# Performance work log

Hardware: AMD Instinct MI355X
Metric: run time of the kernel (lower is better)

Reference implementation:

```python
import jax, jax.numpy as jnp
import numpy as np

NUM_HEADS = 16

def setup_inputs() -> dict:
    key = jax.random.key(0)
    ks = jax.random.split(key, 6)
    C = 512
    nW, B, N = 64, 4, 144
    x = jax.random.normal(ks[0], (B * nW, N, C), dtype=jnp.float32)
    mask = jax.random.randint(ks[1], (nW, N, N), 0, 2, dtype=jnp.int32)
    Wqkv = jax.random.normal(ks[2], (C, 3 * C), dtype=jnp.float32) * (1.0 / np.sqrt(C))
    bqkv = jnp.zeros((3 * C,), dtype=jnp.float32)
    Wproj = jax.random.normal(ks[3], (C, C), dtype=jnp.float32) * (1.0 / np.sqrt(C))
    bproj = jnp.zeros((C,), dtype=jnp.float32)
    return {"x": x, "mask": mask, "Wqkv": Wqkv, "bqkv": bqkv, "Wproj": Wproj, "bproj": bproj}

def reference(x, mask, Wqkv, bqkv, Wproj, bproj):
    Bn, N, C = x.shape
    H = NUM_HEADS
    D = C // H
    nW = mask.shape[0]
    B = Bn // nW
    scale = 1.0 / jnp.sqrt(jnp.asarray(D, dtype=x.dtype))

    qkv = x @ Wqkv + bqkv                        # (Bn, N, 3C)
    qkv = qkv.reshape(Bn, N, 3, H, D)            # packed order (qkv, H, D)
    qkv = jnp.transpose(qkv, (2, 0, 3, 1, 4))    # (3, Bn, H, N, D)
    q, k, v = qkv[0], qkv[1], qkv[2]

    # split window-batch dim: (B nW) -> B, nW
    q = q.reshape(B, nW, H, N, D)
    k = k.reshape(B, nW, H, N, D)
    v = v.reshape(B, nW, H, N, D)

    attn = jnp.einsum('bwhnd,bwhmd->bwhnm', q, k) * scale
    bias = jnp.where(mask == 0, -jnp.inf, 0.0).astype(x.dtype)  # (nW, N, N)
    attn = attn + bias.reshape(1, nW, 1, N, N)
    attn = jax.nn.softmax(attn, axis=-1)

    out = jnp.einsum('bwhnm,bwhmd->bwhnd', attn, v)   # (B, nW, H, N, D)
    out = jnp.transpose(out, (0, 1, 3, 2, 4)).reshape(Bn, N, C)
    return out @ Wproj + bproj
```

## Files before the change

kernel.cpp:

```cpp
#include <hip/hip_runtime.h>

typedef unsigned short u16;
typedef unsigned int u32;
typedef __attribute__((ext_vector_type(4))) float f32x4;
typedef __attribute__((ext_vector_type(8))) short bf16x8;
typedef __attribute__((ext_vector_type(4))) u32 u32x4;

__device__ __forceinline__ u16 f2bf(float f) {
  union { float f; u32 u; } v; v.f = f;
  u32 r = v.u + 0x7fffu + ((v.u >> 16) & 1u);
  return (u16)(r >> 16);
}

__device__ __forceinline__ u16 f2bf_rne(float f) {
  u32 w;
  asm("v_cvt_pk_bf16_f32 %0, %1, %2" : "=v"(w) : "v"(f), "v"(f));
  return (u16)w;
}

__device__ __forceinline__ void gload_lds16(const u16* g, u16* l) {
  __builtin_amdgcn_global_load_lds((__attribute__((address_space(1))) const void*)g,
                                   (__attribute__((address_space(3))) void*)l,
                                   16, 0, 0);
}

__global__ void __launch_bounds__(256) k_transpose_w(const float* __restrict__ W,
                                                     u16* __restrict__ Wt, int K, int Nc) {
  __shared__ u16 t[64][72];
  const int tid = threadIdx.x;
  const int kb = blockIdx.x * 64, nb = blockIdx.y * 64;
  const int c4 = (tid & 15) * 4;
  const int r0 = tid >> 4;
#pragma unroll
  for (int rr = 0; rr < 4; ++rr) {
    int r = rr * 16 + r0;
    float4 v = *(const float4*)(W + (size_t)(kb + r) * Nc + nb + c4);
    t[r][c4 + 0] = f2bf(v.x);
    t[r][c4 + 1] = f2bf(v.y);
    t[r][c4 + 2] = f2bf(v.z);
    t[r][c4 + 3] = f2bf(v.w);
  }
  __syncthreads();
  const int c8 = (tid & 7) * 8;
  const int rn = tid >> 3;
#pragma unroll
  for (int rr = 0; rr < 2; ++rr) {
    int n = rr * 32 + rn;
    u16 tmp[8];
#pragma unroll
    for (int j = 0; j < 8; ++j) tmp[j] = t[c8 + j][n];
    *(u32x4*)(Wt + (size_t)(nb + n) * K + kb + c8) = *(const u32x4*)tmp;
  }
}

__global__ void k_mask_bits(const int* __restrict__ mask, u32* __restrict__ mtab) {
  int idx = blockIdx.x * blockDim.x + threadIdx.x;
  if (idx >= 64 * 144 * 8) return;
  int wd = idx & 7;
  int r = idx >> 3;
  u32 bits = 0;
  if (wd < 5) {
    int base = r * 144 + wd * 32;
    int nmax = 144 - wd * 32;
    if (nmax > 32) nmax = 32;
    for (int b = 0; b < nmax; ++b) bits |= (mask[base + b] ? 1u : 0u) << b;
  }
  mtab[idx] = bits;
}

template <bool OUT_BF16, bool A_FP32>
__global__ void __launch_bounds__(256, 3) k_gemm(const void* __restrict__ Ap,
                                                 const u16* __restrict__ Bt,
                                                 const float* __restrict__ bias,
                                                 void* __restrict__ D,
                                                 int Nc, int K, int NB) {
  __shared__ u16 As[128 * 68];
  __shared__ u16 Bs[2][128 * 64];
  const int tid = threadIdx.x;
  const int wave = tid >> 6, lane = tid & 63;
  const int wr = wave >> 1, wc = wave & 1;
  const int l15 = lane & 15, g = lane >> 4;
  const int sx = l15 & 7;
  const f32x4 fzero = {0.f, 0.f, 0.f, 0.f};

  const int cpx = gridDim.x >> 3;
  const int swz = (blockIdx.x & 7) * cpx + (blockIdx.x >> 3);
  const int bm = swz / NB, bn = swz % NB;

  const u16* Bb = Bt + (size_t)bn * 128 * K;

  int rr[4], cc[4];
#pragma unroll
  for (int i = 0; i < 4; ++i) {
    int e = i * 256 + tid;
    rr[i] = e >> 3;
    cc[i] = e & 7;
  }

  f32x4 acc[4][4];
#pragma unroll
  for (int m = 0; m < 4; ++m)
#pragma unroll
    for (int n = 0; n < 4; ++n) acc[m][n] = fzero;

  f32x4 areg[8];
  u32x4 aregb[4];

  auto A_LOAD = [&](int ks) {
    if constexpr (A_FP32) {
      const float* Af = (const float*)Ap;
#pragma unroll
      for (int i = 0; i < 4; ++i) {
        const float* p = Af + (size_t)(bm * 128 + rr[i]) * K + ks + cc[i] * 8;
        areg[2 * i] = *(const f32x4*)(p);
        areg[2 * i + 1] = *(const f32x4*)(p + 4);
      }
    } else {
      const u16* Ab = (const u16*)Ap + (size_t)bm * 128 * K;
#pragma unroll
      for (int i = 0; i < 4; ++i)
        aregb[i] = *(const u32x4*)(Ab + (size_t)rr[i] * K + ks + cc[i] * 8);
    }
  };

  auto A_WRITE = [&]() {
#pragma unroll
    for (int i = 0; i < 4; ++i) {
      u32x4 wv;
      if constexpr (A_FP32) {
        u32 w0, w1, w2, w3;
        asm("v_cvt_pk_bf16_f32 %0, %1, %2" : "=v"(w0) : "v"(areg[2 * i][0]), "v"(areg[2 * i][1]));
        asm("v_cvt_pk_bf16_f32 %0, %1, %2" : "=v"(w1) : "v"(areg[2 * i][2]), "v"(areg[2 * i][3]));
        asm("v_cvt_pk_bf16_f32 %0, %1, %2" : "=v"(w2) : "v"(areg[2 * i + 1][0]), "v"(areg[2 * i + 1][1]));
        asm("v_cvt_pk_bf16_f32 %0, %1, %2" : "=v"(w3) : "v"(areg[2 * i + 1][2]), "v"(areg[2 * i + 1][3]));
        wv[0] = w0; wv[1] = w1; wv[2] = w2; wv[3] = w3;
      } else {
        wv = aregb[i];
      }
      *(u32x4*)(&As[rr[i] * 68 + cc[i] * 8]) = wv;
    }
  };

  auto B_STAGE = [&](int buf, int ks) {
#pragma unroll
    for (int i = 0; i < 4; ++i) {
      int cs = cc[i] ^ (rr[i] & 7);
      gload_lds16(Bb + (size_t)rr[i] * K + ks + (cs << 3), &Bs[buf][(i * 256 + tid) * 8]);
    }
  };

  auto COMPUTE = [&](int buf) {
#pragma unroll
    for (int kk = 0; kk < 2; ++kk) {
      bf16x8 a[4], b[4];
#pragma unroll
      for (int m = 0; m < 4; ++m)
        a[m] = *(const bf16x8*)(&As[(wr * 64 + m * 16 + l15) * 68 + (kk * 4 + g) * 8]);
#pragma unroll
      for (int n = 0; n < 4; ++n)
        b[n] = *(const bf16x8*)(&Bs[buf][(wc * 64 + n * 16 + l15) * 64 + (((kk * 4 + g) ^ sx) << 3)]);
#pragma unroll
      for (int m = 0; m < 4; ++m)
#pragma unroll
        for (int n = 0; n < 4; ++n)
          acc[m][n] = __builtin_amdgcn_mfma_f32_16x16x32_bf16(a[m], b[n], acc[m][n], 0, 0, 0);
    }
  };

  const int nt = K >> 6;
  A_LOAD(0);
  B_STAGE(0, 0);
  int cur = 0;
  for (int t = 0; t < nt; ++t) {
    asm volatile("s_waitcnt vmcnt(0)" ::: "memory");
    __builtin_amdgcn_sched_barrier(0);
    if (t + 1 < nt) B_STAGE(cur ^ 1, (t + 1) << 6);
    A_WRITE();
    if (t + 1 < nt) A_LOAD((t + 1) << 6);
    asm volatile("s_waitcnt lgkmcnt(0)" ::: "memory");
    __builtin_amdgcn_sched_barrier(0);
    __builtin_amdgcn_s_barrier();
    __builtin_amdgcn_sched_barrier(0);
    COMPUTE(cur);
    __builtin_amdgcn_sched_barrier(0);
    if (t + 1 < nt) __builtin_amdgcn_s_barrier();
    cur ^= 1;
  }

  const int row0 = bm * 128 + wr * 64;
  const int col0 = bn * 128 + wc * 64;
#pragma unroll
  for (int m = 0; m < 4; ++m) {
#pragma unroll
    for (int n = 0; n < 4; ++n) {
      int col = col0 + n * 16 + l15;
      float bv = bias[col];
#pragma unroll
      for (int j = 0; j < 4; ++j) {
        int row = row0 + m * 16 + g * 4 + j;
        float v = acc[m][n][j] + bv;
        if constexpr (OUT_BF16)
          ((u16*)D)[(size_t)row * Nc + col] = f2bf_rne(v);
        else
          ((float*)D)[(size_t)row * Nc + col] = v;
      }
    }
  }
}

__global__ void __launch_bounds__(192) k_attn(const u16* __restrict__ qkv,
                                              const u32* __restrict__ mtab,
                                              u16* __restrict__ obuf) {
  __shared__ u16 k_s[144 * 40];
  __shared__ u16 vT_s[32 * 168];
  __shared__ u16 P_s[3][16 * 168];

  const int bh = blockIdx.x;
  const int bn = bh >> 4, h = bh & 15;
  const int wid = bn & 63;
  const int tid = threadIdx.x;
  const int wave = tid >> 6, lane = tid & 63;
  const int l15 = lane & 15, g = lane >> 4;
  const f32x4 fzero = {0.f, 0.f, 0.f, 0.f};

  const u16* base = qkv + (size_t)bn * 144 * 1536 + h * 32;
  u16* Pw = &P_s[wave][0];

  bf16x8 qb[3];
  u32 mw[3][5];
#pragma unroll
  for (int it = 0; it < 3; ++it) {
    const int mt = wave + it * 3;
    qb[it] = *(const bf16x8*)(base + (size_t)(mt * 16 + l15) * 1536 + g * 8);
    const u32* mp = mtab + ((size_t)(wid * 144 + mt * 16 + l15) << 3);
#pragma unroll
    for (int wd = 0; wd < 5; ++wd) mw[it][wd] = mp[wd];
  }

  *(u32*)(Pw + l15 * 168 + 144 + g * 4) = 0;
  *(u32*)(Pw + l15 * 168 + 144 + g * 4 + 2) = 0;

  for (int e = tid; e < 576; e += 192) {
    int n = e >> 2, c = e & 3;
    const u16* rowp = base + (size_t)n * 1536 + c * 8;
    u32x4 kv = *(const u32x4*)(rowp + 512);
    u32x4 vv = *(const u32x4*)(rowp + 1024);
    *(u32x4*)(k_s + n * 40 + c * 8) = kv;
#pragma unroll
    for (int t = 0; t < 4; ++t) {
      u32 w = vv[t];
      vT_s[(c * 8 + 2 * t) * 168 + n] = (u16)(w & 0xffffu);
      vT_s[(c * 8 + 2 * t + 1) * 168 + n] = (u16)(w >> 16);
    }
  }
  for (int e = tid; e < 512; e += 192) {
    int d = e >> 4, c = e & 15;
    vT_s[d * 168 + 144 + c] = 0;
  }
  __syncthreads();

  const float scale = 0.17677669529663687f;

#pragma unroll
  for (int it = 0; it < 3; ++it) {
    const int mt = wave + it * 3;

    f32x4 accs[9];
#pragma unroll
    for (int nt = 0; nt < 9; ++nt) {
      bf16x8 kf = *(const bf16x8*)(k_s + (nt * 16 + l15) * 40 + g * 8);
      accs[nt] = __builtin_amdgcn_mfma_f32_16x16x32_bf16(kf, qb[it], fzero, 0, 0, 0);
    }

    float rsum = 0.f;
#pragma unroll
    for (int nt = 0; nt < 9; ++nt) {
      const int wd = nt >> 1;
      const int shb = (nt & 1) * 16;
#pragma unroll
      for (int j = 0; j < 4; ++j) {
        float e = __expf(accs[nt][j] * scale);
        u32 bit = (mw[it][wd] >> (shb + g * 4 + j)) & 1u;
        e = bit ? e : 0.f;
        accs[nt][j] = e;
        rsum += e;
      }
    }
    rsum += __shfl_xor(rsum, 16, 64);
    rsum += __shfl_xor(rsum, 32, 64);
    const float rinv = 1.f / rsum;

#pragma unroll
    for (int nt = 0; nt < 9; ++nt) {
      u32 w0, w1;
      float p0 = accs[nt][0] * rinv, p1 = accs[nt][1] * rinv;
      float p2 = accs[nt][2] * rinv, p3 = accs[nt][3] * rinv;
      asm("v_cvt_pk_bf16_f32 %0, %1, %2" : "=v"(w0) : "v"(p0), "v"(p1));
      asm("v_cvt_pk_bf16_f32 %0, %1, %2" : "=v"(w1) : "v"(p2), "v"(p3));
      *(u32*)(Pw + l15 * 168 + nt * 16 + g * 4) = w0;
      *(u32*)(Pw + l15 * 168 + nt * 16 + g * 4 + 2) = w1;
    }

    asm volatile("s_waitcnt lgkmcnt(0)" ::: "memory");
    __builtin_amdgcn_sched_barrier(0);

    f32x4 acco[2];
    acco[0] = fzero;
    acco[1] = fzero;
#pragma unroll
    for (int kk = 0; kk < 5; ++kk) {
      bf16x8 pa = *(const bf16x8*)(Pw + l15 * 168 + kk * 32 + g * 8);
#pragma unroll
      for (int nt2 = 0; nt2 < 2; ++nt2) {
        bf16x8 b = *(const bf16x8*)(vT_s + (nt2 * 16 + l15) * 168 + kk * 32 + g * 8);
        acco[nt2] = __builtin_amdgcn_mfma_f32_16x16x32_bf16(pa, b, acco[nt2], 0, 0, 0);
      }
    }
#pragma unroll
    for (int nt2 = 0; nt2 < 2; ++nt2)
#pragma unroll
      for (int j = 0; j < 4; ++j) {
        int r = mt * 16 + g * 4 + j;
        int d = nt2 * 16 + l15;
        obuf[((size_t)bn * 144 + r) * 512 + h * 32 + d] = f2bf_rne(acco[nt2][j]);
      }
  }
}

extern "C" void kernel_launch(void* const* d_in, const int* in_sizes, int n_in,
                              void* d_out, int out_size, void* d_ws, size_t ws_size,
                              hipStream_t stream) {
  const float* x = (const float*)d_in[0];
  const int* mask = (const int*)d_in[1];
  const float* Wqkv = (const float*)d_in[2];
  const float* bqkv = (const float*)d_in[3];
  const float* Wproj = (const float*)d_in[4];
  const float* bproj = (const float*)d_in[5];
  float* out = (float*)d_out;

  char* ws = (char*)d_ws;
  u32* mtab    = (u32*)(ws + 0);
  u16* wqkv_t  = (u16*)(ws + 294912);
  u16* qkv     = (u16*)(ws + 1867776);
  u16* obuf    = (u16*)(ws + 115113984);
  u16* wproj_t = (u16*)(ws + 152862720);

  k_transpose_w<<<dim3(8, 24), 256, 0, stream>>>(Wqkv, wqkv_t, 512, 1536);
  k_transpose_w<<<dim3(8, 8), 256, 0, stream>>>(Wproj, wproj_t, 512, 512);
  k_mask_bits<<<288, 256, 0, stream>>>(mask, mtab);
  k_gemm<true, true><<<3456, 256, 0, stream>>>(x, wqkv_t, bqkv, qkv, 1536, 512, 12);
  k_attn<<<4096, 192, 0, stream>>>(qkv, mtab, obuf);
  k_gemm<false, false><<<1152, 256, 0, stream>>>(obuf, wproj_t, bproj, out, 512, 512, 4);
}
```

Measured before the change: 196.9 us.

## Use nine waves per attention block and ballot-based mask bit packing

The attention kernel now launches 576 threads (9 waves) per window-head, so each wave handles a single 16-row query tile instead of looping over three. K/V staging is done in one pass, with one row chunk per thread. The mask bitpacking kernel uses wave ballots over rows instead of serial per-thread loops. MFMA priority is raised around the PV product. The larger blocks raise per-block LDS use (9 P buffers), which may limit how many blocks fit per CU.

```diff
diff --git a/kernel.cpp b/kernel.cpp
--- a/kernel.cpp
+++ b/kernel.cpp
@@ -2,6 +2,7 @@
 
 typedef unsigned short u16;
 typedef unsigned int u32;
+typedef unsigned long long u64;
 typedef __attribute__((ext_vector_type(4))) float f32x4;
 typedef __attribute__((ext_vector_type(8))) short bf16x8;
 typedef __attribute__((ext_vector_type(4))) u32 u32x4;
@@ -53,19 +54,21 @@
   }
 }
 
-__global__ void k_mask_bits(const int* __restrict__ mask, u32* __restrict__ mtab) {
-  int idx = blockIdx.x * blockDim.x + threadIdx.x;
-  if (idx >= 64 * 144 * 8) return;
-  int wd = idx & 7;
-  int r = idx >> 3;
-  u32 bits = 0;
-  if (wd < 5) {
-    int base = r * 144 + wd * 32;
-    int nmax = 144 - wd * 32;
-    if (nmax > 32) nmax = 32;
-    for (int b = 0; b < nmax; ++b) bits |= (mask[base + b] ? 1u : 0u) << b;
-  }
-  mtab[idx] = bits;
+__global__ void __launch_bounds__(256) k_mask_bits(const int* __restrict__ mask,
+                                                   u32* __restrict__ mtab) {
+  const int row = blockIdx.x * 4 + (threadIdx.x >> 6);
+  const int lane = threadIdx.x & 63;
+  const int* base = mask + (size_t)row * 144;
+  u64 b01 = __ballot(base[lane] != 0);
+  u64 b23 = __ballot(base[64 + lane] != 0);
+  int v4 = (lane < 16) ? base[128 + lane] : 0;
+  u64 b4 = __ballot(v4 != 0);
+  if (lane == 0) {
+    u32* o = mtab + (size_t)row * 8;
+    o[0] = (u32)b01; o[1] = (u32)(b01 >> 32);
+    o[2] = (u32)b23; o[3] = (u32)(b23 >> 32);
+    o[4] = (u32)b4;  o[5] = 0; o[6] = 0; o[7] = 0;
+  }
 }
 
 template <bool OUT_BF16, bool A_FP32>
@@ -208,12 +211,12 @@
   }
 }
 
-__global__ void __launch_bounds__(192) k_attn(const u16* __restrict__ qkv,
+__global__ void __launch_bounds__(576) k_attn(const u16* __restrict__ qkv,
                                               const u32* __restrict__ mtab,
                                               u16* __restrict__ obuf) {
   __shared__ u16 k_s[144 * 40];
   __shared__ u16 vT_s[32 * 168];
-  __shared__ u16 P_s[3][16 * 168];
+  __shared__ u16 P_s[9][16 * 168];
 
   const int bh = blockIdx.x;
   const int bn = bh >> 4, h = bh & 15;
@@ -225,23 +228,19 @@
 
   const u16* base = qkv + (size_t)bn * 144 * 1536 + h * 32;
   u16* Pw = &P_s[wave][0];
-
-  bf16x8 qb[3];
-  u32 mw[3][5];
-#pragma unroll
-  for (int it = 0; it < 3; ++it) {
-    const int mt = wave + it * 3;
-    qb[it] = *(const bf16x8*)(base + (size_t)(mt * 16 + l15) * 1536 + g * 8);
-    const u32* mp = mtab + ((size_t)(wid * 144 + mt * 16 + l15) << 3);
-#pragma unroll
-    for (int wd = 0; wd < 5; ++wd) mw[it][wd] = mp[wd];
-  }
+  const int mt = wave;
+
+  bf16x8 qb = *(const bf16x8*)(base + (size_t)(mt * 16 + l15) * 1536 + g * 8);
+  const u32* mp = mtab + ((size_t)(wid * 144 + mt * 16 + l15) << 3);
+  u32 mw[5];
+#pragma unroll
+  for (int wd = 0; wd < 5; ++wd) mw[wd] = mp[wd];
 
   *(u32*)(Pw + l15 * 168 + 144 + g * 4) = 0;
   *(u32*)(Pw + l15 * 168 + 144 + g * 4 + 2) = 0;
 
-  for (int e = tid; e < 576; e += 192) {
-    int n = e >> 2, c = e & 3;
+  {
+    const int n = tid >> 2, c = tid & 3;
     const u16* rowp = base + (size_t)n * 1536 + c * 8;
     u32x4 kv = *(const u32x4*)(rowp + 512);
     u32x4 vv = *(const u32x4*)(rowp + 1024);
@@ -253,78 +252,76 @@
       vT_s[(c * 8 + 2 * t + 1) * 168 + n] = (u16)(w >> 16);
     }
   }
-  for (int e = tid; e < 512; e += 192) {
-    int d = e >> 4, c = e & 15;
+  if (tid < 512) {
+    int d = tid >> 4, c = tid & 15;
     vT_s[d * 168 + 144 + c] = 0;
   }
   __syncthreads();
 
   const float scale = 0.17677669529663687f;
 
-#pragma unroll
-  for (int it = 0; it < 3; ++it) {
-    const int mt = wave + it * 3;
-
-    f32x4 accs[9];
-#pragma unroll
-    for (int nt = 0; nt < 9; ++nt) {
-      bf16x8 kf = *(const bf16x8*)(k_s + (nt * 16 + l15) * 40 + g * 8);
-      accs[nt] = __builtin_amdgcn_mfma_f32_16x16x32_bf16(kf, qb[it], fzero, 0, 0, 0);
-    }
-
-    float rsum = 0.f;
-#pragma unroll
-    for (int nt = 0; nt < 9; ++nt) {
-      const int wd = nt >> 1;
-      const int shb = (nt & 1) * 16;
-#pragma unroll
-      for (int j = 0; j < 4; ++j) {
-        float e = __expf(accs[nt][j] * scale);
-        u32 bit = (mw[it][wd] >> (shb + g * 4 + j)) & 1u;
-        e = bit ? e : 0.f;
-        accs[nt][j] = e;
-        rsum += e;
-      }
-    }
-    rsum += __shfl_xor(rsum, 16, 64);
-    rsum += __shfl_xor(rsum, 32, 64);
-    const float rinv = 1.f / rsum;
-
-#pragma unroll
-    for (int nt = 0; nt < 9; ++nt) {
-      u32 w0, w1;
-      float p0 = accs[nt][0] * rinv, p1 = accs[nt][1] * rinv;
-      float p2 = accs[nt][2] * rinv, p3 = accs[nt][3] * rinv;
-      asm("v_cvt_pk_bf16_f32 %0, %1, %2" : "=v"(w0) : "v"(p0), "v"(p1));
-      asm("v_cvt_pk_bf16_f32 %0, %1, %2" : "=v"(w1) : "v"(p2), "v"(p3));
-      *(u32*)(Pw + l15 * 168 + nt * 16 + g * 4) = w0;
-      *(u32*)(Pw + l15 * 168 + nt * 16 + g * 4 + 2) = w1;
-    }
-
-    asm volatile("s_waitcnt lgkmcnt(0)" ::: "memory");
-    __builtin_amdgcn_sched_barrier(0);
-
-    f32x4 acco[2];
-    acco[0] = fzero;
-    acco[1] = fzero;
-#pragma unroll
-    for (int kk = 0; kk < 5; ++kk) {
-      bf16x8 pa = *(const bf16x8*)(Pw + l15 * 168 + kk * 32 + g * 8);
-#pragma unroll
-      for (int nt2 = 0; nt2 < 2; ++nt2) {
-        bf16x8 b = *(const bf16x8*)(vT_s + (nt2 * 16 + l15) * 168 + kk * 32 + g * 8);
-        acco[nt2] = __builtin_amdgcn_mfma_f32_16x16x32_bf16(pa, b, acco[nt2], 0, 0, 0);
-      }
-    }
-#pragma unroll
-    for (int nt2 = 0; nt2 < 2; ++nt2)
-#pragma unroll
-      for (int j = 0; j < 4; ++j) {
-        int r = mt * 16 + g * 4 + j;
-        int d = nt2 * 16 + l15;
-        obuf[((size_t)bn * 144 + r) * 512 + h * 32 + d] = f2bf_rne(acco[nt2][j]);
-      }
-  }
+  f32x4 accs[9];
+#pragma unroll
+  for (int nt = 0; nt < 9; ++nt) {
+    bf16x8 kf = *(const bf16x8*)(k_s + (nt * 16 + l15) * 40 + g * 8);
+    accs[nt] = __builtin_amdgcn_mfma_f32_16x16x32_bf16(kf, qb, fzero, 0, 0, 0);
+  }
+
+  float rsum = 0.f;
+#pragma unroll
+  for (int nt = 0; nt < 9; ++nt) {
+    const int wd = nt >> 1;
+    const int shb = (nt & 1) * 16;
+#pragma unroll
+    for (int j = 0; j < 4; ++j) {
+      float e = __expf(accs[nt][j] * scale);
+      u32 bit = (mw[wd] >> (shb + g * 4 + j)) & 1u;
+      e = bit ? e : 0.f;
+      accs[nt][j] = e;
+      rsum += e;
+    }
+  }
+  rsum += __shfl_xor(rsum, 16, 64);
+  rsum += __shfl_xor(rsum, 32, 64);
+  const float rinv = 1.f / rsum;
+
+#pragma unroll
+  for (int nt = 0; nt < 9; ++nt) {
+    u32 w0, w1;
+    float p0 = accs[nt][0] * rinv, p1 = accs[nt][1] * rinv;
+    float p2 = accs[nt][2] * rinv, p3 = accs[nt][3] * rinv;
+    asm("v_cvt_pk_bf16_f32 %0, %1, %2" : "=v"(w0) : "v"(p0), "v"(p1));
+    asm("v_cvt_pk_bf16_f32 %0, %1, %2" : "=v"(w1) : "v"(p2), "v"(p3));
+    *(u32*)(Pw + l15 * 168 + nt * 16 + g * 4) = w0;
+    *(u32*)(Pw + l15 * 168 + nt * 16 + g * 4 + 2) = w1;
+  }
+
+  asm volatile("s_waitcnt lgkmcnt(0)" ::: "memory");
+  __builtin_amdgcn_sched_barrier(0);
+
+  f32x4 acco[2];
+  acco[0] = fzero;
+  acco[1] = fzero;
+  __builtin_amdgcn_s_setprio(1);
+#pragma unroll
+  for (int kk = 0; kk < 5; ++kk) {
+    bf16x8 pa = *(const bf16x8*)(Pw + l15 * 168 + kk * 32 + g * 8);
+#pragma unroll
+    for (int nt2 = 0; nt2 < 2; ++nt2) {
+      bf16x8 b = *(const bf16x8*)(vT_s + (nt2 * 16 + l15) * 168 + kk * 32 + g * 8);
+      acco[nt2] = __builtin_amdgcn_mfma_f32_16x16x32_bf16(pa, b, acco[nt2], 0, 0, 0);
+    }
+  }
+  __builtin_amdgcn_s_setprio(0);
+
+#pragma unroll
+  for (int nt2 = 0; nt2 < 2; ++nt2)
+#pragma unroll
+    for (int j = 0; j < 4; ++j) {
+      int r = mt * 16 + g * 4 + j;
+      int d = nt2 * 16 + l15;
+      obuf[((size_t)bn * 144 + r) * 512 + h * 32 + d] = f2bf_rne(acco[nt2][j]);
+    }
 }
 
 extern "C" void kernel_launch(void* const* d_in, const int* in_sizes, int n_in,
@@ -347,8 +344,8 @@
 
   k_transpose_w<<<dim3(8, 24), 256, 0, stream>>>(Wqkv, wqkv_t, 512, 1536);
   k_transpose_w<<<dim3(8, 8), 256, 0, stream>>>(Wproj, wproj_t, 512, 512);
-  k_mask_bits<<<288, 256, 0, stream>>>(mask, mtab);
+  k_mask_bits<<<2304, 256, 0, stream>>>(mask, mtab);
   k_gemm<true, true><<<3456, 256, 0, stream>>>(x, wqkv_t, bqkv, qkv, 1536, 512, 12);
-  k_attn<<<4096, 192, 0, stream>>>(qkv, mtab, obuf);
+  k_attn<<<4096, 576, 0, stream>>>(qkv, mtab, obuf);
   k_gemm<false, false><<<1152, 256, 0, stream>>>(obuf, wproj_t, bproj, out, 512, 512, 4);
 }
```

Result: slower. 207.9 us (+5.6%).
